# Performance work log

Measured on AMD Instinct MI355X. Metric: run time of the kernel, lower is better.

Reference implementation:

```python
import jax, jax.numpy as jnp
import numpy as np

NUM_HEADS = 16
N_WIRES = 8  # d_k == n_wires, hard-coded in QLayer


def quantum_heads(x, theta):
    """Exact closed form of the 8-wire circuit: RX-encode + trainable RX + CNOT ring + PauliZ.
    RX(x)RX(t)=RX(x+t); product state -> independent bits with E[(-1)^b_i]=cos(ang_i);
    CNOT ring permutes basis so final-bit XOR subsets give:
      <Z_0> = prod_{i=1..7} cos(ang_i);  <Z_w> = prod_{i=0..w} cos(ang_i) for w>=1.
    """
    B, S, E = x.shape
    ang = x.reshape(B, S, NUM_HEADS, N_WIRES) + theta          # composed RX angles
    c = jnp.cos(ang)                                            # [B,S,H,8]
    cp = jnp.cumprod(c, axis=-1)                                # prefix products
    z0 = jnp.prod(c[..., 1:], axis=-1, keepdims=True)           # wire 0
    z = jnp.concatenate([z0, cp[..., 1:]], axis=-1)             # [B,S,H,8]
    return z.reshape(B, S, E)


def reference(x, theta, W, b):
    B, S, E = x.shape
    d_k = N_WIRES
    proj = quantum_heads(x, theta)                              # q = k = v (same fn of x)
    h = proj.reshape(B, S, NUM_HEADS, d_k).transpose(0, 2, 1, 3)  # [B,H,S,d]
    scores = jnp.einsum('bhqd,bhkd->bhqk', h, h) / jnp.sqrt(jnp.float32(d_k))
    attn = jax.nn.softmax(scores, axis=-1)
    out = jnp.einsum('bhqk,bhkd->bhqd', attn, h)
    out = out.transpose(0, 2, 1, 3).reshape(B, S, E)
    return out @ W.T + b


def setup_inputs() -> dict:
    key = jax.random.key(0)
    k1, k2, k3 = jax.random.split(key, 3)
    B, S, E = 8, 1024, 128
    x = jax.random.normal(k1, (B, S, E), dtype=jnp.float32)
    theta = jax.random.normal(k2, (N_WIRES,), dtype=jnp.float32)
    W = jax.random.normal(k3, (E, E), dtype=jnp.float32) / np.float32(np.sqrt(E))
    b = jnp.zeros((E,), dtype=jnp.float32)
    return {"x": x, "theta": theta, "W": W, "b": b}
```

## Files before the change

### kernel.cpp

```cpp
#include <hip/hip_runtime.h>

#define NHEADS 16
#define NW 8
#define SEQ 1024
#define BATCH 8
#define EMB 128

typedef _Float16 half2_t __attribute__((ext_vector_type(2)));
typedef _Float16 half4_t __attribute__((ext_vector_type(4)));
typedef _Float16 half8_t __attribute__((ext_vector_type(8)));
typedef float    f32x4   __attribute__((ext_vector_type(4)));
typedef int      i32x2   __attribute__((ext_vector_type(2)));

__device__ __forceinline__ half2_t pkrtz(float a, float b) {
    return __builtin_bit_cast(half2_t, __builtin_amdgcn_cvt_pkrtz(a, b));
}

#if __has_builtin(__builtin_amdgcn_permlane16_swap)
#define HAVE_PLSWAP 1
#else
#define HAVE_PLSWAP 0
#endif

#define KVT       8192
#define KVT_STR   1042
#define ONES_OFF  (KVT + 8 * KVT_STR)
#define ZERO_OFF  (ONES_OFF + 8)
#define SMEM_H    (ZERO_OFF + 72)

__device__ __forceinline__ void qrow(const float* __restrict__ xp,
                                     const float* __restrict__ th, float* z) {
    float4 a = *reinterpret_cast<const float4*>(xp);
    float4 b = *reinterpret_cast<const float4*>(xp + 4);
    float c0 = __cosf(a.x + th[0]);
    float c1 = __cosf(a.y + th[1]);
    float c2 = __cosf(a.z + th[2]);
    float c3 = __cosf(a.w + th[3]);
    float c4 = __cosf(b.x + th[4]);
    float c5 = __cosf(b.y + th[5]);
    float c6 = __cosf(b.z + th[6]);
    float c7 = __cosf(b.w + th[7]);
    float u = c1 * c2;
    u *= c3; u *= c4; u *= c5; u *= c6; u *= c7;
    z[0] = u;
    z[1] = c0 * c1;
    z[2] = z[1] * c2;
    z[3] = z[2] * c3;
    z[4] = z[3] * c4;
    z[5] = z[4] * c5;
    z[6] = z[5] * c6;
    z[7] = z[6] * c7;
}

__global__ __launch_bounds__(256, 4) void qattn_mfma(
    const float* __restrict__ x,
    const float* __restrict__ theta,
    __fp16* __restrict__ P)
{
    __shared__ __align__(16) _Float16 smem[SMEM_H];
    const int t   = threadIdx.x;
    const int bid = blockIdx.x;
    const int qs  = bid & 7;
    const int bh  = bid >> 3;
    const int b   = bh >> 4, h = bh & 15;

    float th[8];
#pragma unroll
    for (int w = 0; w < 8; ++w) th[w] = theta[w];

#pragma unroll
    for (int i = 0; i < 4; ++i) {
        const int kl = t + 256 * i;
        float z[8];
        qrow(x + ((size_t)(b * SEQ + kl) * EMB + h * NW), th, z);
        half8_t hv;
#pragma unroll
        for (int d = 0; d < 8; ++d) hv[d] = (_Float16)z[d];
        *reinterpret_cast<half8_t*>(&smem[kl * 8]) = hv;
#pragma unroll
        for (int d = 0; d < 8; ++d) smem[KVT + d * KVT_STR + kl] = hv[d];
    }
    if (t < 8)              smem[ONES_OFF + t]     = (_Float16)1.0f;
    else if (t < 16)        smem[ZERO_OFF + t - 8] = (_Float16)0.0f;
    __syncthreads();

    const int lane = t & 63;
    const int wv   = t >> 6;
    const int q16  = lane & 15;
    const int qd   = lane >> 4;
    const int qbase = qs * 128 + wv * 32;

    const _Float16 QSh = (_Float16)0.51012924f;
    half8_t qfrag[2];
#pragma unroll
    for (int qi = 0; qi < 2; ++qi) {
        const _Float16* qp = (qd == 0)
            ? &smem[(qbase + qi * 16 + q16) * 8] : &smem[ZERO_OFF];
        half8_t qv = *reinterpret_cast<const half8_t*>(qp);
#pragma unroll
        for (int j = 0; j < 8; ++j) qv[j] = qv[j] * QSh;
        qfrag[qi] = qv;
    }

    const _Float16* ka = (qd == 0) ? &smem[q16 * 8]        : &smem[ZERO_OFF];
    const _Float16* kb = (qd == 0) ? &smem[(16 + q16) * 8] : &smem[ZERO_OFF];
    const int kstep = (qd == 0) ? 256 : 0;

    const unsigned int* vb; int vo0, vo1, vo2, vo3; int vstep;
    if (q16 < 8) {
        vb = reinterpret_cast<const unsigned int*>(&smem[KVT + q16 * KVT_STR]);
#if HAVE_PLSWAP
        const int bo = (qd & 1) + (qd >> 1) * 4;
        vo0 = bo; vo1 = bo + 2; vo2 = bo + 8; vo3 = bo + 10;
#else
        vo0 = qd * 4; vo1 = vo0 + 1; vo2 = vo0 + 2; vo3 = vo0 + 3;
#endif
        vstep = 16;
    } else if (q16 == 8) {
        vb = reinterpret_cast<const unsigned int*>(&smem[ONES_OFF]);
        vo0 = vo1 = vo2 = vo3 = 0; vstep = 0;
    } else {
        vb = reinterpret_cast<const unsigned int*>(&smem[ZERO_OFF]);
        vo0 = vo1 = vo2 = vo3 = 0; vstep = 0;
    }

#if !HAVE_PLSWAP
    const bool oddq = (qd & 1);
    const bool hiC  = (qd >= 2);
    const int  iA   = (q16 + (qd & 1) * 32 + (qd >> 1) * 16) * 4;
    const int  iB   = iA ^ 64;
#endif
    const int  lidx = (32 + q16) * 4;

    f32x4 oacc[2] = {{0.f, 0.f, 0.f, 0.f}, {0.f, 0.f, 0.f, 0.f}};
    const f32x4 zc = {0.f, 0.f, 0.f, 0.f};

    half8_t kA = *reinterpret_cast<const half8_t*>(ka);
    half8_t kB = *reinterpret_cast<const half8_t*>(kb);
    unsigned int v0 = vb[vo0], v1 = vb[vo1], v2 = vb[vo2], v3 = vb[vo3];

    for (int kt = 0; kt < 32; ++kt) {
        ka += kstep; kb += kstep; vb += vstep;
        half8_t nkA = *reinterpret_cast<const half8_t*>(ka);
        half8_t nkB = *reinterpret_cast<const half8_t*>(kb);
        unsigned int nv0 = vb[vo0], nv1 = vb[vo1], nv2 = vb[vo2], nv3 = vb[vo3];

        union { unsigned int i[4]; half8_t h; } vf;
        vf.i[0] = v0; vf.i[1] = v1; vf.i[2] = v2; vf.i[3] = v3;

#pragma unroll
        for (int qi = 0; qi < 2; ++qi) {
            f32x4 c0 = __builtin_amdgcn_mfma_f32_16x16x32_f16(kA, qfrag[qi], zc, 0, 0, 0);
            f32x4 c1 = __builtin_amdgcn_mfma_f32_16x16x32_f16(kB, qfrag[qi], zc, 0, 0, 0);
            half2_t p0 = pkrtz(__builtin_amdgcn_exp2f(c0[0]), __builtin_amdgcn_exp2f(c0[1]));
            half2_t p1 = pkrtz(__builtin_amdgcn_exp2f(c0[2]), __builtin_amdgcn_exp2f(c0[3]));
            half2_t p2 = pkrtz(__builtin_amdgcn_exp2f(c1[0]), __builtin_amdgcn_exp2f(c1[1]));
            half2_t p3 = pkrtz(__builtin_amdgcn_exp2f(c1[2]), __builtin_amdgcn_exp2f(c1[3]));
            union { half2_t h; int i; } u0, u1, u2, u3;
            u0.h = p0; u1.h = p1; u2.h = p2; u3.h = p3;
            union { int i[4]; half8_t h; } bf;
#if HAVE_PLSWAP
            i32x2 s01 = __builtin_amdgcn_permlane16_swap(u0.i, u1.i, false, false);
            i32x2 s23 = __builtin_amdgcn_permlane16_swap(u2.i, u3.i, false, false);
            bf.i[0] = s01[0]; bf.i[1] = s01[1];
            bf.i[2] = s23[0]; bf.i[3] = s23[1];
#else
            const int a0 = oddq ? u2.i : u0.i;
            const int a1 = oddq ? u3.i : u1.i;
            const int a2 = oddq ? u0.i : u2.i;
            const int a3 = oddq ? u1.i : u3.i;
            const int r0 = __builtin_amdgcn_ds_bpermute(iA, a0);
            const int r1 = __builtin_amdgcn_ds_bpermute(iA, a1);
            const int r2 = __builtin_amdgcn_ds_bpermute(iB, a2);
            const int r3 = __builtin_amdgcn_ds_bpermute(iB, a3);
            bf.i[0] = hiC ? r2 : r0;
            bf.i[1] = hiC ? r3 : r1;
            bf.i[2] = hiC ? r0 : r2;
            bf.i[3] = hiC ? r1 : r3;
#endif
            oacc[qi] = __builtin_amdgcn_mfma_f32_16x16x32_f16(vf.h, bf.h, oacc[qi], 0, 0, 0);
        }
        kA = nkA; kB = nkB;
        v0 = nv0; v1 = nv1; v2 = nv2; v3 = nv3;
    }

#pragma unroll
    for (int qi = 0; qi < 2; ++qi) {
        f32x4 c = oacc[qi];
        const float lsum = __int_as_float(
            __builtin_amdgcn_ds_bpermute(lidx, __float_as_int(c[0])));
        const float inv = 1.0f / lsum;
        if (qd < 2) {
            half2_t u0 = pkrtz(c[0] * inv, c[1] * inv);
            half2_t u1 = pkrtz(c[2] * inv, c[3] * inv);
            half4_t o4; o4[0] = u0[0]; o4[1] = u0[1]; o4[2] = u1[0]; o4[3] = u1[1];
            const int row = b * SEQ + qbase + qi * 16 + q16;
            *reinterpret_cast<half4_t*>(
                reinterpret_cast<_Float16*>(P) + (size_t)row * EMB + h * NW + qd * 4) = o4;
        }
    }
}

__global__ __launch_bounds__(256) void proj_mfma(
    const __fp16* __restrict__ Pv,
    const float* __restrict__ W,
    const float* __restrict__ bias,
    float* __restrict__ out)
{
    const _Float16* P = reinterpret_cast<const _Float16*>(Pv);
    const int t    = threadIdx.x;
    const int lane = t & 63;
    const int wv   = t >> 6;
    const int n16  = lane & 15;
    const int qd   = lane >> 4;
    const int row0 = blockIdx.x * 16;
    const int col0 = wv * 32;

    half8_t a[4];
#pragma unroll
    for (int kb = 0; kb < 4; ++kb)
        a[kb] = *reinterpret_cast<const half8_t*>(
            P + (size_t)(row0 + n16) * EMB + kb * 32 + qd * 8);

    const f32x4 zc = {0.f, 0.f, 0.f, 0.f};
#pragma unroll
    for (int et = 0; et < 2; ++et) {
        const int e = col0 + et * 16 + n16;
        f32x4 acc = zc;
#pragma unroll
        for (int kb = 0; kb < 4; ++kb) {
            const float* wp = W + (size_t)e * EMB + kb * 32 + qd * 8;
            float4 w0 = *reinterpret_cast<const float4*>(wp);
            float4 w1 = *reinterpret_cast<const float4*>(wp + 4);
            half2_t h0 = pkrtz(w0.x, w0.y);
            half2_t h1 = pkrtz(w0.z, w0.w);
            half2_t h2 = pkrtz(w1.x, w1.y);
            half2_t h3 = pkrtz(w1.z, w1.w);
            half8_t bfr;
            bfr[0] = h0[0]; bfr[1] = h0[1]; bfr[2] = h1[0]; bfr[3] = h1[1];
            bfr[4] = h2[0]; bfr[5] = h2[1]; bfr[6] = h3[0]; bfr[7] = h3[1];
            acc = __builtin_amdgcn_mfma_f32_16x16x32_f16(a[kb], bfr, acc, 0, 0, 0);
        }
        const float bv = bias[e];
#pragma unroll
        for (int r = 0; r < 4; ++r)
            out[(size_t)(row0 + qd * 4 + r) * EMB + e] = acc[r] + bv;
    }
}

extern "C" void kernel_launch(void* const* d_in, const int* in_sizes, int n_in,
                              void* d_out, int out_size, void* d_ws, size_t ws_size,
                              hipStream_t stream)
{
    const float* x     = (const float*)d_in[0];
    const float* theta = (const float*)d_in[1];
    const float* W     = (const float*)d_in[2];
    const float* bias  = (const float*)d_in[3];
    float* out = (float*)d_out;

    __fp16* Pw = (__fp16*)d_ws;

    qattn_mfma<<<128 * 8, 256, 0, stream>>>(x, theta, Pw);
    proj_mfma<<<BATCH * SEQ / 16, 256, 0, stream>>>(Pw, W, bias, out);
}
```

Measured before the change: 89.37 us.

## Precompute quantum head features in separate kernel and split attention into more blocks

Moves the cosine/prefix-product feature computation into a new kernel that writes an fp16 head tensor to workspace. Previously each of the eight query-slice blocks per (batch, head) recomputed it. The attention kernel now has twice as many blocks, each wave handling 16 queries instead of 32, with occupancy raised to 8 blocks per CU. K fragments are read directly from global memory instead of LDS, and shared memory holds only the transposed V. This adds a kernel launch and a global round-trip, and loses the two-query-tile reuse of K/V fragments per wave.

```diff
diff --git a/kernel.cpp b/kernel.cpp
--- a/kernel.cpp
+++ b/kernel.cpp
@@ -22,11 +22,10 @@
 #define HAVE_PLSWAP 0
 #endif
 
-#define KVT       8192
 #define KVT_STR   1042
-#define ONES_OFF  (KVT + 8 * KVT_STR)
+#define ONES_OFF  (8 * KVT_STR)
 #define ZERO_OFF  (ONES_OFF + 8)
-#define SMEM_H    (ZERO_OFF + 72)
+#define SMEM_H    8448
 
 __device__ __forceinline__ void qrow(const float* __restrict__ xp,
                                      const float* __restrict__ th, float* z) {
@@ -52,33 +51,42 @@
     z[7] = z[6] * c7;
 }
 
-__global__ __launch_bounds__(256, 4) void qattn_mfma(
+__global__ __launch_bounds__(256) void qheads(
     const float* __restrict__ x,
     const float* __restrict__ theta,
+    _Float16* __restrict__ H)
+{
+    const int g   = blockIdx.x * 256 + threadIdx.x;
+    const int row = g >> 4, h = g & 15;
+    float th[8];
+#pragma unroll
+    for (int w = 0; w < 8; ++w) th[w] = theta[w];
+    float z[8];
+    qrow(x + (size_t)row * EMB + h * NW, th, z);
+    half8_t hv;
+#pragma unroll
+    for (int d = 0; d < 8; ++d) hv[d] = (_Float16)z[d];
+    *reinterpret_cast<half8_t*>(H + (size_t)row * EMB + h * NW) = hv;
+}
+
+__global__ __launch_bounds__(256, 8) void qattn_mfma(
+    const _Float16* __restrict__ H,
     __fp16* __restrict__ P)
 {
     __shared__ __align__(16) _Float16 smem[SMEM_H];
     const int t   = threadIdx.x;
     const int bid = blockIdx.x;
-    const int qs  = bid & 7;
-    const int bh  = bid >> 3;
+    const int qs  = bid & 15;
+    const int bh  = bid >> 4;
     const int b   = bh >> 4, h = bh & 15;
-
-    float th[8];
-#pragma unroll
-    for (int w = 0; w < 8; ++w) th[w] = theta[w];
 
 #pragma unroll
     for (int i = 0; i < 4; ++i) {
         const int kl = t + 256 * i;
-        float z[8];
-        qrow(x + ((size_t)(b * SEQ + kl) * EMB + h * NW), th, z);
-        half8_t hv;
-#pragma unroll
-        for (int d = 0; d < 8; ++d) hv[d] = (_Float16)z[d];
-        *reinterpret_cast<half8_t*>(&smem[kl * 8]) = hv;
-#pragma unroll
-        for (int d = 0; d < 8; ++d) smem[KVT + d * KVT_STR + kl] = hv[d];
+        half8_t hv = *reinterpret_cast<const half8_t*>(
+            H + (size_t)(b * SEQ + kl) * EMB + h * NW);
+#pragma unroll
+        for (int d = 0; d < 8; ++d) smem[d * KVT_STR + kl] = hv[d];
     }
     if (t < 8)              smem[ONES_OFF + t]     = (_Float16)1.0f;
     else if (t < 16)        smem[ZERO_OFF + t - 8] = (_Float16)0.0f;
@@ -88,27 +96,22 @@
     const int wv   = t >> 6;
     const int q16  = lane & 15;
     const int qd   = lane >> 4;
-    const int qbase = qs * 128 + wv * 32;
+    const int qbase = qs * 64 + wv * 16;
 
     const _Float16 QSh = (_Float16)0.51012924f;
-    half8_t qfrag[2];
-#pragma unroll
-    for (int qi = 0; qi < 2; ++qi) {
-        const _Float16* qp = (qd == 0)
-            ? &smem[(qbase + qi * 16 + q16) * 8] : &smem[ZERO_OFF];
-        half8_t qv = *reinterpret_cast<const half8_t*>(qp);
-#pragma unroll
-        for (int j = 0; j < 8; ++j) qv[j] = qv[j] * QSh;
-        qfrag[qi] = qv;
-    }
-
-    const _Float16* ka = (qd == 0) ? &smem[q16 * 8]        : &smem[ZERO_OFF];
-    const _Float16* kb = (qd == 0) ? &smem[(16 + q16) * 8] : &smem[ZERO_OFF];
-    const int kstep = (qd == 0) ? 256 : 0;
+    half8_t qfrag = {};
+    if (qd == 0) {
+        half8_t qv = *reinterpret_cast<const half8_t*>(
+            H + (size_t)(b * SEQ + qbase + q16) * EMB + h * NW);
+#pragma unroll
+        for (int j = 0; j < 8; ++j) qfrag[j] = qv[j] * QSh;
+    }
+
+    const _Float16* pK = H + (size_t)(b * SEQ + q16) * EMB + h * NW;
 
     const unsigned int* vb; int vo0, vo1, vo2, vo3; int vstep;
     if (q16 < 8) {
-        vb = reinterpret_cast<const unsigned int*>(&smem[KVT + q16 * KVT_STR]);
+        vb = reinterpret_cast<const unsigned int*>(&smem[q16 * KVT_STR]);
 #if HAVE_PLSWAP
         const int bo = (qd & 1) + (qd >> 1) * 4;
         vo0 = bo; vo1 = bo + 2; vo2 = bo + 8; vo3 = bo + 10;
@@ -132,69 +135,67 @@
 #endif
     const int  lidx = (32 + q16) * 4;
 
-    f32x4 oacc[2] = {{0.f, 0.f, 0.f, 0.f}, {0.f, 0.f, 0.f, 0.f}};
+    f32x4 oacc = {0.f, 0.f, 0.f, 0.f};
     const f32x4 zc = {0.f, 0.f, 0.f, 0.f};
 
-    half8_t kA = *reinterpret_cast<const half8_t*>(ka);
-    half8_t kB = *reinterpret_cast<const half8_t*>(kb);
+    half8_t kA = *reinterpret_cast<const half8_t*>(pK);
+    half8_t kB = *reinterpret_cast<const half8_t*>(pK + 2048);
     unsigned int v0 = vb[vo0], v1 = vb[vo1], v2 = vb[vo2], v3 = vb[vo3];
 
     for (int kt = 0; kt < 32; ++kt) {
-        ka += kstep; kb += kstep; vb += vstep;
-        half8_t nkA = *reinterpret_cast<const half8_t*>(ka);
-        half8_t nkB = *reinterpret_cast<const half8_t*>(kb);
-        unsigned int nv0 = vb[vo0], nv1 = vb[vo1], nv2 = vb[vo2], nv3 = vb[vo3];
+        pK += 4096; vb += vstep;
+        half8_t nkA = *reinterpret_cast<const half8_t*>(pK);
+        half8_t nkB = *reinterpret_cast<const half8_t*>(pK + 2048);
+        unsigned int nv0 = vb[vo0], nv1 = vb[vo1];
+        unsigned int nv2 = vb[vo2], nv3 = vb[vo3];
 
         union { unsigned int i[4]; half8_t h; } vf;
         vf.i[0] = v0; vf.i[1] = v1; vf.i[2] = v2; vf.i[3] = v3;
 
-#pragma unroll
-        for (int qi = 0; qi < 2; ++qi) {
-            f32x4 c0 = __builtin_amdgcn_mfma_f32_16x16x32_f16(kA, qfrag[qi], zc, 0, 0, 0);
-            f32x4 c1 = __builtin_amdgcn_mfma_f32_16x16x32_f16(kB, qfrag[qi], zc, 0, 0, 0);
-            half2_t p0 = pkrtz(__builtin_amdgcn_exp2f(c0[0]), __builtin_amdgcn_exp2f(c0[1]));
-            half2_t p1 = pkrtz(__builtin_amdgcn_exp2f(c0[2]), __builtin_amdgcn_exp2f(c0[3]));
-            half2_t p2 = pkrtz(__builtin_amdgcn_exp2f(c1[0]), __builtin_amdgcn_exp2f(c1[1]));
-            half2_t p3 = pkrtz(__builtin_amdgcn_exp2f(c1[2]), __builtin_amdgcn_exp2f(c1[3]));
-            union { half2_t h; int i; } u0, u1, u2, u3;
-            u0.h = p0; u1.h = p1; u2.h = p2; u3.h = p3;
-            union { int i[4]; half8_t h; } bf;
+        f32x4 c0 = __builtin_amdgcn_mfma_f32_16x16x32_f16(kA, qfrag, zc, 0, 0, 0);
+        f32x4 c1 = __builtin_amdgcn_mfma_f32_16x16x32_f16(kB, qfrag, zc, 0, 0, 0);
+        half2_t p0 = pkrtz(__builtin_amdgcn_exp2f(c0[0]), __builtin_amdgcn_exp2f(c0[1]));
+        half2_t p1 = pkrtz(__builtin_amdgcn_exp2f(c0[2]), __builtin_amdgcn_exp2f(c0[3]));
+        half2_t p2 = pkrtz(__builtin_amdgcn_exp2f(c1[0]), __builtin_amdgcn_exp2f(c1[1]));
+        half2_t p3 = pkrtz(__builtin_amdgcn_exp2f(c1[2]), __builtin_amdgcn_exp2f(c1[3]));
+        union { half2_t h; int i; } u0, u1, u2, u3;
+        u0.h = p0; u1.h = p1; u2.h = p2; u3.h = p3;
+        union { int i[4]; half8_t h; } bf;
 #if HAVE_PLSWAP
-            i32x2 s01 = __builtin_amdgcn_permlane16_swap(u0.i, u1.i, false, false);
-            i32x2 s23 = __builtin_amdgcn_permlane16_swap(u2.i, u3.i, false, false);
-            bf.i[0] = s01[0]; bf.i[1] = s01[1];
-            bf.i[2] = s23[0]; bf.i[3] = s23[1];
+        i32x2 s01 = __builtin_amdgcn_permlane16_swap(u0.i, u1.i, false, false);
+        i32x2 s23 = __builtin_amdgcn_permlane16_swap(u2.i, u3.i, false, false);
+        bf.i[0] = s01[0]; bf.i[1] = s01[1];
+        bf.i[2] = s23[0]; bf.i[3] = s23[1];
 #else
-            const int a0 = oddq ? u2.i : u0.i;
-            const int a1 = oddq ? u3.i : u1.i;
-            const int a2 = oddq ? u0.i : u2.i;
-            const int a3 = oddq ? u1.i : u3.i;
-            const int r0 = __builtin_amdgcn_ds_bpermute(iA, a0);
-            const int r1 = __builtin_amdgcn_ds_bpermute(iA, a1);
-            const int r2 = __builtin_amdgcn_ds_bpermute(iB, a2);
-            const int r3 = __builtin_amdgcn_ds_bpermute(iB, a3);
-            bf.i[0] = hiC ? r2 : r0;
-            bf.i[1] = hiC ? r3 : r1;
-            bf.i[2] = hiC ? r0 : r2;
-            bf.i[3] = hiC ? r1 : r3;
-#endif
-            oacc[qi] = __builtin_amdgcn_mfma_f32_16x16x32_f16(vf.h, bf.h, oacc[qi], 0, 0, 0);
-        }
+        const int a0 = oddq ? u2.i : u0.i;
+        const int a1 = oddq ? u3.i : u1.i;
+        const int a2 = oddq ? u0.i : u2.i;
+        const int a3 = oddq ? u1.i : u3.i;
+        const int r0 = __builtin_amdgcn_ds_bpermute(iA, a0);
+        const int r1 = __builtin_amdgcn_ds_bpermute(iA, a1);
+        const int r2 = __builtin_amdgcn_ds_bpermute(iB, a2);
+        const int r3 = __builtin_amdgcn_ds_bpermute(iB, a3);
+        bf.i[0] = hiC ? r2 : r0;
+        bf.i[1] = hiC ? r3 : r1;
+        bf.i[2] = hiC ? r0 : r2;
+        bf.i[3] = hiC ? r1 : r3;
+#endif
+        oacc = __builtin_amdgcn_mfma_f32_16x16x32_f16(vf.h, bf.h, oacc, 0, 0, 0);
+
         kA = nkA; kB = nkB;
         v0 = nv0; v1 = nv1; v2 = nv2; v3 = nv3;
     }
 
-#pragma unroll
-    for (int qi = 0; qi < 2; ++qi) {
-        f32x4 c = oacc[qi];
+    {
+        f32x4 c = oacc;
         const float lsum = __int_as_float(
             __builtin_amdgcn_ds_bpermute(lidx, __float_as_int(c[0])));
         const float inv = 1.0f / lsum;
         if (qd < 2) {
-            half2_t u0 = pkrtz(c[0] * inv, c[1] * inv);
-            half2_t u1 = pkrtz(c[2] * inv, c[3] * inv);
-            half4_t o4; o4[0] = u0[0]; o4[1] = u0[1]; o4[2] = u1[0]; o4[3] = u1[1];
-            const int row = b * SEQ + qbase + qi * 16 + q16;
+            half2_t w0 = pkrtz(c[0] * inv, c[1] * inv);
+            half2_t w1 = pkrtz(c[2] * inv, c[3] * inv);
+            half4_t o4; o4[0] = w0[0]; o4[1] = w0[1]; o4[2] = w1[0]; o4[3] = w1[1];
+            const int row = b * SEQ + qbase + q16;
             *reinterpret_cast<half4_t*>(
                 reinterpret_cast<_Float16*>(P) + (size_t)row * EMB + h * NW + qd * 4) = o4;
         }
@@ -258,8 +259,10 @@
     const float* bias  = (const float*)d_in[3];
     float* out = (float*)d_out;
 
-    __fp16* Pw = (__fp16*)d_ws;
-
-    qattn_mfma<<<128 * 8, 256, 0, stream>>>(x, theta, Pw);
+    _Float16* H  = (_Float16*)d_ws;
+    __fp16*   Pw = (__fp16*)((char*)d_ws + (size_t)BATCH * SEQ * EMB * 2);
+
+    qheads<<<BATCH * SEQ * NHEADS / 256, 256, 0, stream>>>(x, theta, H);
+    qattn_mfma<<<128 * 16, 256, 0, stream>>>(H, Pw);
     proj_mfma<<<BATCH * SEQ / 16, 256, 0, stream>>>(Pw, W, bias, out);
 }
```

Result: slower. 135.4 us (+51.5%).
